# Kernel optimization log

Measured on AMD Instinct MI355X. Metric: run time of the kernel, lower is better.

The kernel has to match this reference:

```python
import jax, jax.numpy as jnp
import numpy as np


def setup_inputs() -> dict:
    key = jax.random.key(0)
    ks = jax.random.split(key, 8)
    B, C, H, W = 4, 256, 64, 64
    C8 = C // 8
    s = 0.05
    return {
        "x": jax.random.normal(ks[0], (B, C, H, W), jnp.float32),
        "wq": jax.random.normal(ks[1], (C8, C), jnp.float32) * s,
        "bq": jax.random.normal(ks[2], (C8,), jnp.float32) * s,
        "wk": jax.random.normal(ks[3], (C8, C), jnp.float32) * s,
        "bk": jax.random.normal(ks[4], (C8,), jnp.float32) * s,
        "wv": jax.random.normal(ks[5], (C, C), jnp.float32) * s,
        "bv": jax.random.normal(ks[6], (C,), jnp.float32) * s,
        "gamma": jax.random.uniform(ks[7], (1,), jnp.float32),
    }


def reference(x, wq, bq, wk, bk, wv, bv, gamma):
    B, C, H, W = x.shape
    N = H * W
    xf = x.reshape(B, C, N)  # flatten spatial: [B, C, N]
    # 1x1 convs are channel-wise matmuls
    q = jnp.einsum("dc,bcn->bnd", wq, xf) + bq[None, None, :]  # [B, N, C/8]
    k = jnp.einsum("dc,bcn->bdn", wk, xf) + bk[None, :, None]  # [B, C/8, N]
    v = jnp.einsum("dc,bcn->bdn", wv, xf) + bv[None, :, None]  # [B, C, N]
    energy = jnp.einsum("bnd,bdm->bnm", q, k)  # [B, N, N]
    attention = jax.nn.softmax(energy, axis=-1)
    # out = value @ attention^T  -> [B, C, N]
    out = jnp.einsum("bcm,bnm->bcn", v, attention)
    out = out.reshape(B, C, H, W)
    return gamma[0] * out + x
```

## Files before the change

kernel.cpp:

```cpp
#include <hip/hip_runtime.h>
#include <hip/hip_bf16.h>
#include <stdint.h>

#define B_ 4
#define C_ 256
#define N_ 4096
#define D_ 32
#define KT 256

typedef __bf16 bf16_t;
typedef __bf16 bf16x4_t __attribute__((ext_vector_type(4)));
typedef __bf16 bf16x8_t __attribute__((ext_vector_type(8)));
typedef float  f32x4    __attribute__((ext_vector_type(4)));

__device__ __forceinline__ void gld_lds16(const void* g, void* l) {
  __builtin_amdgcn_global_load_lds((__attribute__((address_space(1))) void*)g,
                                   (__attribute__((address_space(3))) void*)l, 16, 0, 0);
}

__global__ __launch_bounds__(256) void cast_w_kernel(
    const float* __restrict__ wq, const float* __restrict__ wk,
    const float* __restrict__ wv, bf16_t* __restrict__ Wb)
{
  const int gr = blockIdx.x;
  const int k  = threadIdx.x;
  float v;
  if (gr < 32)      v = wq[gr * C_ + k];
  else if (gr < 64) v = wk[(gr - 32) * C_ + k];
  else              v = wv[(gr - 64) * C_ + k];
  Wb[gr * C_ + k] = (bf16_t)v;
}

__global__ __launch_bounds__(256) void cast_x_kernel(
    const float* __restrict__ x, bf16_t* __restrict__ xbT)
{
  __shared__ float xs[64][65];
  const int n0 = blockIdx.x * 64;
  const int c0 = blockIdx.y * 64;
  const int b  = blockIdx.z;
  const int t  = threadIdx.x;

  const int lr = t >> 4;
  const int lc = (t & 15) * 4;
#pragma unroll
  for (int i = 0; i < 4; ++i) {
    const f32x4 v = *(const f32x4*)(x + ((size_t)(b * C_ + c0 + lr + i * 16)) * N_ + n0 + lc);
    xs[lr + i * 16][lc + 0] = v[0];
    xs[lr + i * 16][lc + 1] = v[1];
    xs[lr + i * 16][lc + 2] = v[2];
    xs[lr + i * 16][lc + 3] = v[3];
  }
  __syncthreads();
  const int nr = t >> 2;
  const int cb = (t & 3) * 16;
  bf16_t tmp[16];
#pragma unroll
  for (int j = 0; j < 16; ++j) tmp[j] = (bf16_t)xs[cb + j][nr];
  bf16_t* dst = xbT + ((size_t)(b * N_ + n0 + nr)) * C_ + c0 + cb;
  *(bf16x8_t*)dst       = *(bf16x8_t*)&tmp[0];
  *(bf16x8_t*)(dst + 8) = *(bf16x8_t*)&tmp[8];
}

__global__ __launch_bounds__(256) void proj_kernel(
    const bf16_t* __restrict__ Wb, const bf16_t* __restrict__ xbT,
    const float* __restrict__ bq, const float* __restrict__ bk,
    const float* __restrict__ bv,
    bf16_t* __restrict__ Qh, bf16_t* __restrict__ Kh, bf16_t* __restrict__ Vh)
{
  const int bi = blockIdx.x;
  const int b  = bi & 3;
  const int n0 = (bi >> 2) * 64;
  const int t = threadIdx.x, w = t >> 6, lane = t & 63;
  const int l4 = lane >> 4, lm = lane & 15;

  const f32x4 z4 = {0.f, 0.f, 0.f, 0.f};
  f32x4 acc[5][4];
#pragma unroll
  for (int rt = 0; rt < 5; ++rt)
#pragma unroll
    for (int ct = 0; ct < 4; ++ct) acc[rt][ct] = z4;

#pragma unroll 1
  for (int k0 = 0; k0 < C_; k0 += 64) {
    bf16x8_t af[5][2], bfr[4][2];
#pragma unroll
    for (int rt = 0; rt < 5; ++rt)
#pragma unroll
      for (int kc = 0; kc < 2; ++kc)
        af[rt][kc] = *(const bf16x8_t*)(Wb + (size_t)(w * 80 + rt * 16 + lm) * C_ + k0 + kc * 32 + l4 * 8);
#pragma unroll
    for (int ct = 0; ct < 4; ++ct)
#pragma unroll
      for (int kc = 0; kc < 2; ++kc)
        bfr[ct][kc] = *(const bf16x8_t*)(xbT + ((size_t)(b * N_ + n0 + ct * 16 + lm)) * C_ + k0 + kc * 32 + l4 * 8);
#pragma unroll
    for (int rt = 0; rt < 5; ++rt)
#pragma unroll
      for (int ct = 0; ct < 4; ++ct)
#pragma unroll
        for (int kc = 0; kc < 2; ++kc)
          acc[rt][ct] = __builtin_amdgcn_mfma_f32_16x16x32_bf16(af[rt][kc], bfr[ct][kc], acc[rt][ct], 0, 0, 0);
  }

#pragma unroll
  for (int rt = 0; rt < 5; ++rt)
#pragma unroll
    for (int r = 0; r < 4; ++r) {
      const int gr = w * 80 + rt * 16 + 4 * l4 + r;
      const float bias = (gr < 32) ? bq[gr] : (gr < 64) ? bk[gr - 32] : bv[gr - 64];
#pragma unroll
      for (int ct = 0; ct < 4; ++ct) {
        const int n = n0 + ct * 16 + lm;
        float v = acc[rt][ct][r] + bias;
        if (gr < 32) {
          v *= 1.44269504088896f;
          Qh[((size_t)(b * N_ + n)) * D_ + gr] = (bf16_t)v;
        } else if (gr < 64) {
          Kh[((size_t)(b * N_ + n)) * D_ + (gr - 32)] = (bf16_t)v;
        } else {
          Vh[((size_t)(b * C_ + (gr - 64))) * N_ + n] = (bf16_t)v;
        }
      }
    }
}

__global__ __launch_bounds__(512, 2) void attn_kernel(
    const bf16_t* __restrict__ Qh, const bf16_t* __restrict__ Kh,
    const bf16_t* __restrict__ Vh, const float* __restrict__ x,
    const float* __restrict__ gamma, float* __restrict__ out)
{
  __shared__ __align__(16) bf16_t Vt[2][C_][64];
  __shared__ __align__(16) bf16_t Pl[2][32][KT];
  __shared__ __align__(16) float  PMx[2][64][4];
  __shared__ __align__(16) float  PSx[2][64][4];

  const int bi = blockIdx.x;
  const int xcd = bi & 7, slot = bi >> 3;
  const int b  = xcd >> 1;
  const int q0 = ((xcd & 1) * 32 + slot) * 64;

  const int t = threadIdx.x, wid = t >> 6, lane = t & 63;
  const int l4 = lane >> 4, lm = lane & 15;
  const int rh = wid & 1, cg = wid >> 1;
  const int pswz = (lm & 7) << 3;

  const f32x4 z4 = {0.f, 0.f, 0.f, 0.f};

  const int vr  = lane >> 3;
  const int msw = ((lane & 7) ^ vr) << 3;
  const bf16_t* vsrc[4];
#pragma unroll
  for (int u = 0; u < 4; ++u)
    vsrc[u] = Vh + ((size_t)(b * C_ + 32 * wid + 8 * u + vr)) * N_ + msw;
#pragma unroll
  for (int u = 0; u < 4; ++u)
    gld_lds16(vsrc[u], &Vt[0][32 * wid + 8 * u][0]);

  const bf16_t* kbase = Kh + ((size_t)(b * N_ + cg * 64 + lm)) * D_ + l4 * 8;
  bf16x8_t kf[4], kn[4];
#pragma unroll
  for (int mt = 0; mt < 4; ++mt)
    kf[mt] = *(const bf16x8_t*)(kbase + (size_t)(mt * 16) * D_);

  bf16x8_t qf[2];
#pragma unroll
  for (int rt2 = 0; rt2 < 2; ++rt2)
    qf[rt2] = *(const bf16x8_t*)(Qh + ((size_t)(b * N_ + q0 + rh * 32 + rt2 * 16 + lm)) * D_ + l4 * 8);

  f32x4 acc[2][4];
#pragma unroll
  for (int rt2 = 0; rt2 < 2; ++rt2)
#pragma unroll
    for (int ct = 0; ct < 4; ++ct) acc[rt2][ct] = z4;
  float m_run[2] = {-1e30f, -1e30f}, l_run[2] = {0.f, 0.f};

  int cur = 0;
#pragma unroll 1
  for (int it = 0; it < N_ / KT; ++it) {
    f32x4 S[2][4];
#pragma unroll
    for (int rt2 = 0; rt2 < 2; ++rt2)
#pragma unroll
      for (int mt = 0; mt < 4; ++mt)
        S[rt2][mt] = __builtin_amdgcn_mfma_f32_16x16x32_bf16(kf[mt], qf[rt2], z4, 0, 0, 0);

    const int k0n = ((it + 1) * KT) & (N_ - 1);
#pragma unroll
    for (int mt = 0; mt < 4; ++mt)
      kn[mt] = *(const bf16x8_t*)(kbase + (size_t)(k0n + mt * 16) * D_);

    float pmx[2];
#pragma unroll
    for (int rt2 = 0; rt2 < 2; ++rt2) {
      float a0 = fmaxf(fmaxf(S[rt2][0][0], S[rt2][0][1]), fmaxf(S[rt2][0][2], S[rt2][0][3]));
      float a1 = fmaxf(fmaxf(S[rt2][1][0], S[rt2][1][1]), fmaxf(S[rt2][1][2], S[rt2][1][3]));
      float a2 = fmaxf(fmaxf(S[rt2][2][0], S[rt2][2][1]), fmaxf(S[rt2][2][2], S[rt2][2][3]));
      float a3 = fmaxf(fmaxf(S[rt2][3][0], S[rt2][3][1]), fmaxf(S[rt2][3][2], S[rt2][3][3]));
      float v = fmaxf(fmaxf(a0, a1), fmaxf(a2, a3));
      v = fmaxf(v, __shfl_xor(v, 16));
      v = fmaxf(v, __shfl_xor(v, 32));
      pmx[rt2] = v;
    }
    if (lane < 32) PMx[rh][lane][cg] = (lane < 16) ? pmx[0] : pmx[1];
    __syncthreads();

    float sc[2], nm[2]; int chg[2];
#pragma unroll
    for (int rt2 = 0; rt2 < 2; ++rt2) {
      const f32x4 pv = *(const f32x4*)&PMx[rh][rt2 * 16 + lm][0];
      const float tm = fmaxf(fmaxf(pv[0], pv[1]), fmaxf(pv[2], pv[3]));
      const float mo = m_run[rt2];
      nm[rt2]  = fmaxf(mo, tm);
      chg[rt2] = tm > mo;
      sc[rt2]  = __builtin_amdgcn_exp2f(mo - nm[rt2]);
      m_run[rt2] = nm[rt2];
    }

    float psx[2];
#pragma unroll
    for (int rt2 = 0; rt2 < 2; ++rt2) {
      float s = 0.f;
      const int prow = rt2 * 16 + lm;
#pragma unroll
      for (int mt = 0; mt < 4; ++mt) {
        const float p0 = __builtin_amdgcn_exp2f(S[rt2][mt][0] - nm[rt2]);
        const float p1 = __builtin_amdgcn_exp2f(S[rt2][mt][1] - nm[rt2]);
        const float p2 = __builtin_amdgcn_exp2f(S[rt2][mt][2] - nm[rt2]);
        const float p3 = __builtin_amdgcn_exp2f(S[rt2][mt][3] - nm[rt2]);
        s += (p0 + p1) + (p2 + p3);
        bf16x4_t w4 = {(bf16_t)p0, (bf16_t)p1, (bf16_t)p2, (bf16_t)p3};
        *(bf16x4_t*)&Pl[rh][prow][(cg * 64 + 16 * mt + 4 * l4) ^ pswz] = w4;
      }
      s += __shfl_xor(s, 16);
      s += __shfl_xor(s, 32);
      psx[rt2] = s;
    }
    if (lane < 32) PSx[rh][lane][cg] = (lane < 16) ? psx[0] : psx[1];

    if (__any(chg[0] || chg[1])) {
#pragma unroll
      for (int rt2 = 0; rt2 < 2; ++rt2)
#pragma unroll
        for (int ct = 0; ct < 4; ++ct) acc[rt2][ct] *= sc[rt2];
    }
    __syncthreads();

#pragma unroll
    for (int rt2 = 0; rt2 < 2; ++rt2) {
      const f32x4 sv = *(const f32x4*)&PSx[rh][rt2 * 16 + lm][0];
      l_run[rt2] = l_run[rt2] * sc[rt2] + ((sv[0] + sv[1]) + (sv[2] + sv[3]));
    }

#pragma unroll 1
    for (int s4 = 0; s4 < 4; ++s4) {
      const int knx = (it * KT + (s4 + 1) * 64) & (N_ - 1);
#pragma unroll
      for (int u = 0; u < 4; ++u)
        gld_lds16(vsrc[u] + knx, &Vt[cur ^ 1][32 * wid + 8 * u][0]);

      bf16x8_t pa[2][2];
#pragma unroll
      for (int rt2 = 0; rt2 < 2; ++rt2)
#pragma unroll
        for (int kc = 0; kc < 2; ++kc)
          pa[rt2][kc] = *(const bf16x8_t*)&Pl[rh][rt2 * 16 + lm][(s4 * 64 + kc * 32 + 8 * l4) ^ pswz];
#pragma unroll
      for (int ct = 0; ct < 4; ++ct) {
#pragma unroll
        for (int kc = 0; kc < 2; ++kc) {
          const bf16x8_t vf = *(const bf16x8_t*)&Vt[cur][cg * 64 + ct * 16 + lm][(kc * 32 + 8 * l4) ^ pswz];
#pragma unroll
          for (int rt2 = 0; rt2 < 2; ++rt2)
            acc[rt2][ct] = __builtin_amdgcn_mfma_f32_16x16x32_bf16(vf, pa[rt2][kc], acc[rt2][ct], 0, 0, 0);
        }
      }
      __syncthreads();
      cur ^= 1;
    }

#pragma unroll
    for (int mt = 0; mt < 4; ++mt) kf[mt] = kn[mt];
  }

  const float g = gamma[0];
  const int n = q0 + rh * 32 + lm;
#pragma unroll
  for (int rt2 = 0; rt2 < 2; ++rt2) {
    const float inv = 1.f / l_run[rt2];
#pragma unroll
    for (int ct = 0; ct < 4; ++ct) {
#pragma unroll
      for (int r = 0; r < 4; ++r) {
        const int c = cg * 64 + ct * 16 + 4 * l4 + r;
        const size_t idx = ((size_t)(b * C_ + c)) * N_ + n + rt2 * 16;
        out[idx] = g * (acc[rt2][ct][r] * inv) + x[idx];
      }
    }
  }
}

extern "C" void kernel_launch(void* const* d_in, const int* in_sizes, int n_in,
                              void* d_out, int out_size, void* d_ws, size_t ws_size,
                              hipStream_t stream) {
  const float* x     = (const float*)d_in[0];
  const float* wq    = (const float*)d_in[1];
  const float* bq    = (const float*)d_in[2];
  const float* wk    = (const float*)d_in[3];
  const float* bk    = (const float*)d_in[4];
  const float* wv    = (const float*)d_in[5];
  const float* bv    = (const float*)d_in[6];
  const float* gamma = (const float*)d_in[7];
  float* out = (float*)d_out;

  bf16_t* Qh  = (bf16_t*)d_ws;
  bf16_t* Kh  = Qh + (size_t)B_ * N_ * D_;
  bf16_t* Vh  = Kh + (size_t)B_ * N_ * D_;
  bf16_t* Wb  = Vh + (size_t)B_ * C_ * N_;
  bf16_t* xbT = Wb + (size_t)320 * C_;

  cast_w_kernel<<<320, 256, 0, stream>>>(wq, wk, wv, Wb);
  cast_x_kernel<<<dim3(64, 4, 4), 256, 0, stream>>>(x, xbT);
  proj_kernel<<<256, 256, 0, stream>>>(Wb, xbT, bq, bk, bv, Qh, Kh, Vh);
  attn_kernel<<<256, 512, 0, stream>>>(Qh, Kh, Vh, x, gamma, out);
}
```

Before: 115.6 us.

## Triple-buffer V tiles with vmcnt-based waits and merge cast kernels

The attention kernel moves from double to triple buffering of V tiles in LDS, prefetching two tiles ahead. It replaces __syncthreads with explicit s_waitcnt vmcnt/lgkmcnt plus s_barrier, so the in-flight global-to-LDS loads for the next tile are not drained at every barrier. The K-fragment prefetch across iterations is dropped in favour of loading K at the top of each iteration, and the inner s4 loop is fully unrolled. The two cast kernels are merged into one launch to save launch overhead. The extra V buffer raises LDS use, which may affect occupancy at two blocks per CU, and the unprefetched K load adds latency at the start of each iteration.

After: 114.6 us. Within noise of the previous version (-0.9%).

```diff
diff --git a/kernel.cpp b/kernel.cpp
--- a/kernel.cpp
+++ b/kernel.cpp
@@ -18,27 +18,27 @@
                                    (__attribute__((address_space(3))) void*)l, 16, 0, 0);
 }
 
-__global__ __launch_bounds__(256) void cast_w_kernel(
+__global__ __launch_bounds__(256) void cast_kernel(
+    const float* __restrict__ x,
     const float* __restrict__ wq, const float* __restrict__ wk,
-    const float* __restrict__ wv, bf16_t* __restrict__ Wb)
+    const float* __restrict__ wv,
+    bf16_t* __restrict__ xbT, bf16_t* __restrict__ Wb)
 {
-  const int gr = blockIdx.x;
-  const int k  = threadIdx.x;
-  float v;
-  if (gr < 32)      v = wq[gr * C_ + k];
-  else if (gr < 64) v = wk[(gr - 32) * C_ + k];
-  else              v = wv[(gr - 64) * C_ + k];
-  Wb[gr * C_ + k] = (bf16_t)v;
-}
-
-__global__ __launch_bounds__(256) void cast_x_kernel(
-    const float* __restrict__ x, bf16_t* __restrict__ xbT)
-{
+  const int bid = blockIdx.x;
+  const int t = threadIdx.x;
+  if (bid >= 1024) {
+    const int gr = bid - 1024;
+    float v;
+    if (gr < 32)      v = wq[gr * C_ + t];
+    else if (gr < 64) v = wk[(gr - 32) * C_ + t];
+    else              v = wv[(gr - 64) * C_ + t];
+    Wb[gr * C_ + t] = (bf16_t)v;
+    return;
+  }
   __shared__ float xs[64][65];
-  const int n0 = blockIdx.x * 64;
-  const int c0 = blockIdx.y * 64;
-  const int b  = blockIdx.z;
-  const int t  = threadIdx.x;
+  const int n0 = (bid & 63) * 64;
+  const int c0 = ((bid >> 6) & 3) * 64;
+  const int b  = bid >> 8;
 
   const int lr = t >> 4;
   const int lc = (t & 15) * 4;
@@ -129,7 +129,7 @@
     const bf16_t* __restrict__ Vh, const float* __restrict__ x,
     const float* __restrict__ gamma, float* __restrict__ out)
 {
-  __shared__ __align__(16) bf16_t Vt[2][C_][64];
+  __shared__ __align__(16) bf16_t Vt[3][C_][64];
   __shared__ __align__(16) bf16_t Pl[2][32][KT];
   __shared__ __align__(16) float  PMx[2][64][4];
   __shared__ __align__(16) float  PSx[2][64][4];
@@ -152,15 +152,13 @@
 #pragma unroll
   for (int u = 0; u < 4; ++u)
     vsrc[u] = Vh + ((size_t)(b * C_ + 32 * wid + 8 * u + vr)) * N_ + msw;
-#pragma unroll
-  for (int u = 0; u < 4; ++u)
-    gld_lds16(vsrc[u], &Vt[0][32 * wid + 8 * u][0]);
+
+#pragma unroll
+  for (int u = 0; u < 4; ++u) gld_lds16(vsrc[u], &Vt[0][32 * wid + 8 * u][0]);
+#pragma unroll
+  for (int u = 0; u < 4; ++u) gld_lds16(vsrc[u] + 64, &Vt[1][32 * wid + 8 * u][0]);
 
   const bf16_t* kbase = Kh + ((size_t)(b * N_ + cg * 64 + lm)) * D_ + l4 * 8;
-  bf16x8_t kf[4], kn[4];
-#pragma unroll
-  for (int mt = 0; mt < 4; ++mt)
-    kf[mt] = *(const bf16x8_t*)(kbase + (size_t)(mt * 16) * D_);
 
   bf16x8_t qf[2];
 #pragma unroll
@@ -174,20 +172,20 @@
     for (int ct = 0; ct < 4; ++ct) acc[rt2][ct] = z4;
   float m_run[2] = {-1e30f, -1e30f}, l_run[2] = {0.f, 0.f};
 
-  int cur = 0;
+  int bufc = 0;
 #pragma unroll 1
   for (int it = 0; it < N_ / KT; ++it) {
+    bf16x8_t kf[4];
+#pragma unroll
+    for (int mt = 0; mt < 4; ++mt)
+      kf[mt] = *(const bf16x8_t*)(kbase + (size_t)(it * KT + mt * 16) * D_);
+
     f32x4 S[2][4];
 #pragma unroll
     for (int rt2 = 0; rt2 < 2; ++rt2)
 #pragma unroll
       for (int mt = 0; mt < 4; ++mt)
         S[rt2][mt] = __builtin_amdgcn_mfma_f32_16x16x32_bf16(kf[mt], qf[rt2], z4, 0, 0, 0);
-
-    const int k0n = ((it + 1) * KT) & (N_ - 1);
-#pragma unroll
-    for (int mt = 0; mt < 4; ++mt)
-      kn[mt] = *(const bf16x8_t*)(kbase + (size_t)(k0n + mt * 16) * D_);
 
     float pmx[2];
 #pragma unroll
@@ -202,7 +200,8 @@
       pmx[rt2] = v;
     }
     if (lane < 32) PMx[rh][lane][cg] = (lane < 16) ? pmx[0] : pmx[1];
-    __syncthreads();
+    asm volatile("s_waitcnt lgkmcnt(0)" ::: "memory");
+    __builtin_amdgcn_s_barrier();
 
     float sc[2], nm[2]; int chg[2];
 #pragma unroll
@@ -243,7 +242,8 @@
 #pragma unroll
         for (int ct = 0; ct < 4; ++ct) acc[rt2][ct] *= sc[rt2];
     }
-    __syncthreads();
+    asm volatile("s_waitcnt lgkmcnt(0)" ::: "memory");
+    __builtin_amdgcn_s_barrier();
 
 #pragma unroll
     for (int rt2 = 0; rt2 < 2; ++rt2) {
@@ -251,12 +251,19 @@
       l_run[rt2] = l_run[rt2] * sc[rt2] + ((sv[0] + sv[1]) + (sv[2] + sv[3]));
     }
 
-#pragma unroll 1
+#pragma unroll
     for (int s4 = 0; s4 < 4; ++s4) {
-      const int knx = (it * KT + (s4 + 1) * 64) & (N_ - 1);
+      if (s4 == 0)
+        asm volatile("s_waitcnt vmcnt(4) lgkmcnt(0)" ::: "memory");
+      else
+        asm volatile("s_waitcnt vmcnt(4)" ::: "memory");
+      __builtin_amdgcn_s_barrier();
+
+      const int knx = (it * KT + (s4 + 2) * 64) & (N_ - 1);
+      const int bst = (bufc < 1) ? bufc + 2 : bufc - 1;
 #pragma unroll
       for (int u = 0; u < 4; ++u)
-        gld_lds16(vsrc[u] + knx, &Vt[cur ^ 1][32 * wid + 8 * u][0]);
+        gld_lds16(vsrc[u] + knx, &Vt[bst][32 * wid + 8 * u][0]);
 
       bf16x8_t pa[2][2];
 #pragma unroll
@@ -268,18 +275,14 @@
       for (int ct = 0; ct < 4; ++ct) {
 #pragma unroll
         for (int kc = 0; kc < 2; ++kc) {
-          const bf16x8_t vf = *(const bf16x8_t*)&Vt[cur][cg * 64 + ct * 16 + lm][(kc * 32 + 8 * l4) ^ pswz];
+          const bf16x8_t vf = *(const bf16x8_t*)&Vt[bufc][cg * 64 + ct * 16 + lm][(kc * 32 + 8 * l4) ^ pswz];
 #pragma unroll
           for (int rt2 = 0; rt2 < 2; ++rt2)
             acc[rt2][ct] = __builtin_amdgcn_mfma_f32_16x16x32_bf16(vf, pa[rt2][kc], acc[rt2][ct], 0, 0, 0);
         }
       }
-      __syncthreads();
-      cur ^= 1;
-    }
-
-#pragma unroll
-    for (int mt = 0; mt < 4; ++mt) kf[mt] = kn[mt];
+      bufc = (bufc == 2) ? 0 : bufc + 1;
+    }
   }
 
   const float g = gamma[0];
@@ -318,8 +321,7 @@
   bf16_t* Wb  = Vh + (size_t)B_ * C_ * N_;
   bf16_t* xbT = Wb + (size_t)320 * C_;
 
-  cast_w_kernel<<<320, 256, 0, stream>>>(wq, wk, wv, Wb);
-  cast_x_kernel<<<dim3(64, 4, 4), 256, 0, stream>>>(x, xbT);
+  cast_kernel<<<1344, 256, 0, stream>>>(x, wq, wk, wv, xbT, Wb);
   proj_kernel<<<256, 256, 0, stream>>>(Wb, xbT, bq, bk, bv, Qh, Kh, Vh);
   attn_kernel<<<256, 512, 0, stream>>>(Qh, Kh, Vh, x, gamma, out);
 }
```
